# Kernel optimization log

Hardware: AMD Instinct MI355X
Metric: run time of the kernel (lower is better)

The kernel has to match this reference:

```python
import jax, jax.numpy as jnp
import numpy as np

N_NODES = 10000
N_MOTIFS = 2500          # N_NODES / subgraph_size(=4)
N_AUG = N_NODES + N_MOTIFS
N_EDGES = 500000
NFEAT = 512
NHID = 128


def setup_inputs() -> dict:
    key = jax.random.key(0)
    ks = jax.random.split(key, 14)
    s = 0.05  # param init scale
    return {
        "x": jax.random.normal(ks[0], (N_NODES, NFEAT), jnp.float32),
        "edge_index": jax.random.randint(ks[1], (2, N_EDGES), 0, N_AUG, jnp.int64),
        "motif_list": jax.random.randint(ks[2], (N_MOTIFS, 4), 0, N_NODES, jnp.int64),
        "W1": jax.random.normal(ks[3], (NFEAT, 2 * NHID), jnp.float32) * s,
        "a_src1": jax.random.normal(ks[4], (2 * NHID,), jnp.float32) * s,
        "a_dst1": jax.random.normal(ks[5], (2 * NHID,), jnp.float32) * s,
        "b1": jnp.zeros((2 * NHID,), jnp.float32),
        "W2": jax.random.normal(ks[6], (2 * NHID, NHID), jnp.float32) * s,
        "a_src2": jax.random.normal(ks[7], (NHID,), jnp.float32) * s,
        "a_dst2": jax.random.normal(ks[8], (NHID,), jnp.float32) * s,
        "b2": jnp.zeros((NHID,), jnp.float32),
        "W_lin": jax.random.normal(ks[9], (NFEAT, NHID), jnp.float32) * s,  # torch Linear(nhid, nfeat) weight
        "b_lin": jnp.zeros((NFEAT,), jnp.float32),
    }


def gat_layer(x, src, dst, W, a_s, a_d, b, n):
    """Single-head GATConv (PyG semantics): edge-softmax attention over dst."""
    h = x @ W                                              # [n, out]
    alpha_s = h @ a_s                                      # [n]
    alpha_d = h @ a_d                                      # [n]
    e = jax.nn.leaky_relu(alpha_s[src] + alpha_d[dst], 0.2)  # [E]
    m = jax.ops.segment_max(e, dst, num_segments=n)        # stable softmax per dst
    w = jnp.exp(e - m[dst])
    denom = jax.ops.segment_sum(w, dst, num_segments=n)
    coef = w / (denom[dst] + 1e-16)                        # [E]
    out = jax.ops.segment_sum(coef[:, None] * h[src], dst, num_segments=n)
    return out + b


def reference(x, edge_index, motif_list, W1, a_src1, a_dst1, b1,
              W2, a_src2, a_dst2, b2, W_lin, b_lin):
    n = x.shape[0] + motif_list.shape[0]
    # augmented features: mean of each motif's node features appended as motif nodes
    x_aug = jnp.concatenate([x, jnp.mean(x[motif_list], axis=1)], axis=0)  # [N_AUG, F]
    # augmented edge list + self loops (GATConv adds self loops)
    loops = jnp.arange(n, dtype=edge_index.dtype)
    src = jnp.concatenate([edge_index[0], loops])
    dst = jnp.concatenate([edge_index[1], loops])
    h1 = gat_layer(x_aug, src, dst, W1, a_src1, a_dst1, b1, n)   # [N_AUG, 2*NHID]
    h2 = gat_layer(h1, src, dst, W2, a_src2, a_dst2, b2, n)      # [N_AUG, NHID]
    rec_adj = jax.nn.sigmoid(h2 @ h2.T)                          # [N_AUG, N_AUG]
    rec_feature = jax.nn.sigmoid(h2 @ W_lin.T + b_lin)           # [N_AUG, NFEAT]
    return (rec_feature, rec_adj)
```

## Files before the change

kernel.cpp:

```cpp
#include <hip/hip_runtime.h>

typedef unsigned short u16;
typedef __attribute__((ext_vector_type(8))) short short8;
typedef __attribute__((ext_vector_type(4))) float f32x4;

#define N_NODES 10000
#define N_MOTIFS 2500
#define N_AUG   12500
#define N_EDGES 500000
#define E_TOT   512500
#define NFEAT   512
#define NH1     256
#define NH2     128

__device__ __forceinline__ float b2f(u16 u){ return __uint_as_float(((unsigned)u) << 16); }
__device__ __forceinline__ u16 f2b(float f){
  unsigned x = __float_as_uint(f);
  x += 0x7fffu + ((x >> 16) & 1u);
  return (u16)(x >> 16);
}

__global__ void k_zero(int* p, int n){
  int i = blockIdx.x * blockDim.x + threadIdx.x;
  if (i < n) p[i] = 0;
}

__global__ void k_xaug(const float* __restrict__ x, const int* __restrict__ motif,
                       u16* __restrict__ xb){
  int gid = blockIdx.x * blockDim.x + threadIdx.x;
  int row = gid >> 6;
  int c   = (gid & 63) << 3;
  if (row >= N_AUG) return;
  float v[8];
  if (row < N_NODES){
    const float* s = &x[(size_t)row * NFEAT + c];
    #pragma unroll
    for (int k = 0; k < 8; ++k) v[k] = s[k];
  } else {
    int m = row - N_NODES;
    const float* p0 = &x[(size_t)motif[m*4+0] * NFEAT + c];
    const float* p1 = &x[(size_t)motif[m*4+1] * NFEAT + c];
    const float* p2 = &x[(size_t)motif[m*4+2] * NFEAT + c];
    const float* p3 = &x[(size_t)motif[m*4+3] * NFEAT + c];
    #pragma unroll
    for (int k = 0; k < 8; ++k) v[k] = (p0[k] + p1[k] + p2[k] + p3[k]) * 0.25f;
  }
  short8 o;
  #pragma unroll
  for (int k = 0; k < 8; ++k) o[k] = (short)f2b(v[k]);
  *(short8*)&xb[(size_t)row * NFEAT + c] = o;
}

__global__ void k_tr(const float* __restrict__ in, u16* __restrict__ out, int R, int C){
  int i = blockIdx.x * blockDim.x + threadIdx.x;
  if (i >= R * C) return;
  int r = i / C, c = i - r * C;
  out[(size_t)c * R + r] = f2b(in[i]);
}

__global__ void k_cvt(const float* __restrict__ in, u16* __restrict__ out, int n){
  int i = blockIdx.x * blockDim.x + threadIdx.x;
  if (i < n) out[i] = f2b(in[i]);
}

__global__ void k_hist(const int* __restrict__ ei, int* __restrict__ cnt){
  int i = blockIdx.x * blockDim.x + threadIdx.x;
  if (i >= E_TOT) return;
  int d = (i < N_EDGES) ? ei[N_EDGES + i] : (i - N_EDGES);
  atomicAdd(&cnt[d], 1);
}

__global__ void k_scan(const int* __restrict__ cnt, int* __restrict__ offs, int* __restrict__ cur){
  __shared__ int part[1024];
  int t = threadIdx.x;
  const int CH = 13;
  int base = t * CH;
  int s = 0;
  for (int i = 0; i < CH; ++i){ int idx = base + i; if (idx < N_AUG) s += cnt[idx]; }
  part[t] = s;
  __syncthreads();
  for (int off = 1; off < 1024; off <<= 1){
    int v = 0;
    if (t >= off) v = part[t - off];
    __syncthreads();
    if (t >= off) part[t] += v;
    __syncthreads();
  }
  int run = (t == 0) ? 0 : part[t - 1];
  for (int i = 0; i < CH; ++i){
    int idx = base + i;
    if (idx <= N_AUG){
      offs[idx] = run;
      if (idx < N_AUG){ cur[idx] = run; run += cnt[idx]; }
    }
  }
}

__global__ void k_scatter(const int* __restrict__ ei, int* __restrict__ cur, int* __restrict__ srcs){
  int i = blockIdx.x * blockDim.x + threadIdx.x;
  if (i >= E_TOT) return;
  int s, d;
  if (i < N_EDGES){ s = ei[i]; d = ei[N_EDGES + i]; } else { s = i - N_EDGES; d = s; }
  int pos = atomicAdd(&cur[d], 1);
  srcs[pos] = s;
}

template<int DIM>
__global__ void k_alpha(const float* __restrict__ h, const float* __restrict__ avs,
                        const float* __restrict__ avd, float* __restrict__ oS, float* __restrict__ oD){
  __shared__ float shS[8], shD[8];
  int n = blockIdx.x, t = threadIdx.x;
  int lane = t & 63, wid = t >> 6;
  float hv = h[(size_t)n * DIM + t];
  float s = hv * avs[t];
  float d = hv * avd[t];
  #pragma unroll
  for (int o = 32; o; o >>= 1){ s += __shfl_down(s, o); d += __shfl_down(d, o); }
  if (lane == 0){ shS[wid] = s; shD[wid] = d; }
  __syncthreads();
  if (t == 0){
    float ss = 0.f, dd = 0.f;
    for (int i = 0; i < DIM/64; ++i){ ss += shS[i]; dd += shD[i]; }
    oS[n] = ss; oD[n] = dd;
  }
}

template<int DIM>
__global__ void k_agg(const int* __restrict__ offs, const int* __restrict__ srcs,
                      const float* __restrict__ aS, const float* __restrict__ aD,
                      const float* __restrict__ hb, const float* __restrict__ bias,
                      u16* __restrict__ hout){
  __shared__ float rsh[8];
  __shared__ float wsh[128];
  __shared__ int   ssh[128];
  int d = blockIdx.x, t = threadIdx.x;
  int lane = t & 63, wid = t >> 6;
  const int NW = DIM / 64;
  int r0 = offs[d], r1 = offs[d + 1];
  float adv = aD[d];

  float mx = -3.0e38f;
  for (int j = r0 + t; j < r1; j += DIM){
    float e = aS[srcs[j]] + adv;
    e = (e >= 0.f) ? e : 0.2f * e;
    mx = fmaxf(mx, e);
  }
  #pragma unroll
  for (int o = 32; o; o >>= 1) mx = fmaxf(mx, __shfl_down(mx, o));
  if (lane == 0) rsh[wid] = mx;
  __syncthreads();
  if (t == 0){ float v = rsh[0]; for (int i = 1; i < NW; ++i) v = fmaxf(v, rsh[i]); rsh[0] = v; }
  __syncthreads();
  mx = rsh[0];
  __syncthreads();

  float sm = 0.f;
  for (int j = r0 + t; j < r1; j += DIM){
    float e = aS[srcs[j]] + adv;
    e = (e >= 0.f) ? e : 0.2f * e;
    sm += __expf(e - mx);
  }
  #pragma unroll
  for (int o = 32; o; o >>= 1) sm += __shfl_down(sm, o);
  if (lane == 0) rsh[wid] = sm;
  __syncthreads();
  if (t == 0){ float v = rsh[0]; for (int i = 1; i < NW; ++i) v += rsh[i]; rsh[0] = v; }
  __syncthreads();
  sm = rsh[0];

  float acc = 0.f;
  for (int base = r0; base < r1; base += 128){
    int cntE = min(128, r1 - base);
    __syncthreads();
    for (int j = t; j < cntE; j += DIM){
      int s = srcs[base + j];
      ssh[j] = s;
      float e = aS[s] + adv;
      e = (e >= 0.f) ? e : 0.2f * e;
      wsh[j] = __expf(e - mx);
    }
    __syncthreads();
    for (int j = 0; j < cntE; ++j)
      acc += wsh[j] * hb[(size_t)ssh[j] * DIM + t];
  }
  float outv = acc / (sm + 1e-16f) + bias[t];
  hout[(size_t)d * DIM + t] = f2b(outv);
}

template<int EPI>
__global__ __launch_bounds__(256) void k_gemm(
    const u16* __restrict__ A, const u16* __restrict__ B,
    float* __restrict__ C, const float* __restrict__ bias,
    int M, int N, int K){
  __shared__ u16 As[128][72];
  __shared__ u16 Bs[128][72];
  int t = threadIdx.x;
  int lane = t & 63, wid = t >> 6;
  int wm = wid >> 1, wn = wid & 1;
  int m0 = blockIdx.y * 128, n0 = blockIdx.x * 128;

  f32x4 acc[4][4];
  #pragma unroll
  for (int i = 0; i < 4; ++i)
    #pragma unroll
    for (int j = 0; j < 4; ++j)
      acc[i][j] = {0.f, 0.f, 0.f, 0.f};

  for (int k0 = 0; k0 < K; k0 += 64){
    __syncthreads();
    #pragma unroll
    for (int i = 0; i < 4; ++i){
      int id = t + i * 256;
      int r = id >> 3, c = (id & 7) << 3;
      int gm = m0 + r; if (gm >= M) gm = M - 1;
      int gn = n0 + r; if (gn >= N) gn = N - 1;
      *(short8*)&As[r][c] = *(const short8*)&A[(size_t)gm * K + k0 + c];
      *(short8*)&Bs[r][c] = *(const short8*)&B[(size_t)gn * K + k0 + c];
    }
    __syncthreads();
    #pragma unroll
    for (int kk = 0; kk < 2; ++kk){
      int kof = kk * 32 + (lane >> 4) * 8;
      short8 af[4], bfr[4];
      #pragma unroll
      for (int mi = 0; mi < 4; ++mi) af[mi]  = *(const short8*)&As[wm*64 + mi*16 + (lane & 15)][kof];
      #pragma unroll
      for (int ni = 0; ni < 4; ++ni) bfr[ni] = *(const short8*)&Bs[wn*64 + ni*16 + (lane & 15)][kof];
      #pragma unroll
      for (int mi = 0; mi < 4; ++mi)
        #pragma unroll
        for (int ni = 0; ni < 4; ++ni)
          acc[mi][ni] = __builtin_amdgcn_mfma_f32_16x16x32_bf16(af[mi], bfr[ni], acc[mi][ni], 0, 0, 0);
    }
  }

  #pragma unroll
  for (int mi = 0; mi < 4; ++mi)
    #pragma unroll
    for (int ni = 0; ni < 4; ++ni){
      int gn = n0 + wn*64 + ni*16 + (lane & 15);
      if (gn >= N) continue;
      #pragma unroll
      for (int r = 0; r < 4; ++r){
        int gm = m0 + wm*64 + mi*16 + (lane >> 4)*4 + r;
        if (gm >= M) continue;
        float v = acc[mi][ni][r];
        if (EPI == 2) v += bias[gn];
        if (EPI >= 1) v = 1.f / (1.f + __expf(-v));
        C[(size_t)gm * N + gn] = v;
      }
    }
}


extern "C" void kernel_launch(void* const* d_in, const int* in_sizes, int n_in,
                              void* d_out, int out_size, void* d_ws, size_t ws_size,
                              hipStream_t stream){
  const float* x    = (const float*)d_in[0];
  const int*   ei   = (const int*)d_in[1];
  const int*   mot  = (const int*)d_in[2];
  const float* W1   = (const float*)d_in[3];
  const float* a_s1 = (const float*)d_in[4];
  const float* a_d1 = (const float*)d_in[5];
  const float* b1   = (const float*)d_in[6];
  const float* W2   = (const float*)d_in[7];
  const float* a_s2 = (const float*)d_in[8];
  const float* a_d2 = (const float*)d_in[9];
  const float* b2   = (const float*)d_in[10];
  const float* Wl   = (const float*)d_in[11];
  const float* bl   = (const float*)d_in[12];

  char* p = (char*)d_ws;
  auto alloc = [&](size_t bytes){ void* r = (void*)p; p += (bytes + 255) & ~(size_t)255; return r; };
  u16*   xaugb = (u16*)alloc((size_t)N_AUG * NFEAT * 2);
  u16*   W1T   = (u16*)alloc((size_t)NH1 * NFEAT * 2);
  u16*   W2T   = (u16*)alloc((size_t)NH2 * NH1 * 2);
  u16*   Wlb   = (u16*)alloc((size_t)NFEAT * NH2 * 2);
  float* h1pre = (float*)alloc((size_t)N_AUG * NH1 * 4);
  u16*   h1out = (u16*)alloc((size_t)N_AUG * NH1 * 2);
  float* h2pre = (float*)alloc((size_t)N_AUG * NH2 * 4);
  u16*   h2b   = (u16*)alloc((size_t)N_AUG * NH2 * 2);
  float* aS    = (float*)alloc((size_t)N_AUG * 4);
  float* aD    = (float*)alloc((size_t)N_AUG * 4);
  int*   cnt   = (int*)alloc((size_t)(N_AUG + 8) * 4);
  int*   offs  = (int*)alloc((size_t)(N_AUG + 8) * 4);
  int*   cur   = (int*)alloc((size_t)(N_AUG + 8) * 4);
  int*   srcs  = (int*)alloc((size_t)E_TOT * 4);

  float* out_feat = (float*)d_out;
  float* out_adj  = out_feat + (size_t)N_AUG * NFEAT;

  k_zero<<<(N_AUG + 8 + 255) / 256, 256, 0, stream>>>(cnt, N_AUG + 8);
  k_xaug<<<(N_AUG * 64 + 255) / 256, 256, 0, stream>>>(x, mot, xaugb);
  k_tr<<<(NFEAT * NH1 + 255) / 256, 256, 0, stream>>>(W1, W1T, NFEAT, NH1);
  k_tr<<<(NH1 * NH2 + 255) / 256, 256, 0, stream>>>(W2, W2T, NH1, NH2);
  k_cvt<<<(NFEAT * NH2 + 255) / 256, 256, 0, stream>>>(Wl, Wlb, NFEAT * NH2);
  k_hist<<<(E_TOT + 255) / 256, 256, 0, stream>>>(ei, cnt);
  k_scan<<<1, 1024, 0, stream>>>(cnt, offs, cur);
  k_scatter<<<(E_TOT + 255) / 256, 256, 0, stream>>>(ei, cur, srcs);

  { dim3 g(NH1 / 128, 98); k_gemm<0><<<g, 256, 0, stream>>>(xaugb, W1T, h1pre, nullptr, N_AUG, NH1, NFEAT); }
  k_alpha<NH1><<<N_AUG, NH1, 0, stream>>>(h1pre, a_s1, a_d1, aS, aD);
  k_agg<NH1><<<N_AUG, NH1, 0, stream>>>(offs, srcs, aS, aD, h1pre, b1, h1out);

  { dim3 g(1, 98); k_gemm<0><<<g, 256, 0, stream>>>(h1out, W2T, h2pre, nullptr, N_AUG, NH2, NH1); }
  k_alpha<NH2><<<N_AUG, NH2, 0, stream>>>(h2pre, a_s2, a_d2, aS, aD);
  k_agg<NH2><<<N_AUG, NH2, 0, stream>>>(offs, srcs, aS, aD, h2pre, b2, h2b);

  { dim3 g(NFEAT / 128, 98); k_gemm<2><<<g, 256, 0, stream>>>(h2b, Wlb, out_feat, bl, N_AUG, NFEAT, NH2); }
  { dim3 g(98, 98);          k_gemm<1><<<g, 256, 0, stream>>>(h2b, h2b, out_adj, nullptr, N_AUG, N_AUG, NH2); }
}
```

Measured before the change: 464.2 us.

## Store GAT hidden features in bf16, pack aggregation to two columns per thread

The projection GEMMs now write bf16 instead of fp32. The alpha and aggregation kernels read bf16, and each aggregation thread handles two packed columns with half as many threads, replacing block reductions with wave shuffles where possible. The weight prep kernels are merged into one launch, and the sigmoid outputs use nontemporal stores. This cuts gather bandwidth in the edge aggregation and some launch overhead, at the cost of lower precision in the attention scores and the aggregated features.

New measurement: 705.7 us, median of 5. +52.0%, slower.

```diff
diff --git a/kernel.cpp b/kernel.cpp
--- a/kernel.cpp
+++ b/kernel.cpp
@@ -1,6 +1,7 @@
 #include <hip/hip_runtime.h>
 
 typedef unsigned short u16;
+typedef unsigned int   u32;
 typedef __attribute__((ext_vector_type(8))) short short8;
 typedef __attribute__((ext_vector_type(4))) float f32x4;
 
@@ -13,16 +14,38 @@
 #define NH1     256
 #define NH2     128
 
-__device__ __forceinline__ float b2f(u16 u){ return __uint_as_float(((unsigned)u) << 16); }
+__device__ __forceinline__ float b2f(u16 u){ return __uint_as_float(((u32)u) << 16); }
 __device__ __forceinline__ u16 f2b(float f){
-  unsigned x = __float_as_uint(f);
+  u32 x = __float_as_uint(f);
   x += 0x7fffu + ((x >> 16) & 1u);
   return (u16)(x >> 16);
 }
 
-__global__ void k_zero(int* p, int n){
+#define PREP_Z   (N_AUG + 8)
+#define PREP_W1  (NFEAT * NH1)
+#define PREP_W2  (NH1 * NH2)
+#define PREP_WL  (NFEAT * NH2)
+#define PREP_TOT (PREP_Z + PREP_W1 + PREP_W2 + PREP_WL)
+
+__global__ void k_prep(const float* __restrict__ W1, const float* __restrict__ W2,
+                       const float* __restrict__ Wl, int* __restrict__ cnt,
+                       u16* __restrict__ W1T, u16* __restrict__ W2T, u16* __restrict__ Wlb){
   int i = blockIdx.x * blockDim.x + threadIdx.x;
-  if (i < n) p[i] = 0;
+  if (i < PREP_Z){ cnt[i] = 0; return; }
+  i -= PREP_Z;
+  if (i < PREP_W1){
+    int r = i / NH1, c = i - r * NH1;
+    W1T[(size_t)c * NFEAT + r] = f2b(W1[i]);
+    return;
+  }
+  i -= PREP_W1;
+  if (i < PREP_W2){
+    int r = i / NH2, c = i - r * NH2;
+    W2T[(size_t)c * NH1 + r] = f2b(W2[i]);
+    return;
+  }
+  i -= PREP_W2;
+  if (i < PREP_WL) Wlb[i] = f2b(Wl[i]);
 }
 
 __global__ void k_xaug(const float* __restrict__ x, const int* __restrict__ motif,
@@ -49,18 +72,6 @@
   #pragma unroll
   for (int k = 0; k < 8; ++k) o[k] = (short)f2b(v[k]);
   *(short8*)&xb[(size_t)row * NFEAT + c] = o;
-}
-
-__global__ void k_tr(const float* __restrict__ in, u16* __restrict__ out, int R, int C){
-  int i = blockIdx.x * blockDim.x + threadIdx.x;
-  if (i >= R * C) return;
-  int r = i / C, c = i - r * C;
-  out[(size_t)c * R + r] = f2b(in[i]);
-}
-
-__global__ void k_cvt(const float* __restrict__ in, u16* __restrict__ out, int n){
-  int i = blockIdx.x * blockDim.x + threadIdx.x;
-  if (i < n) out[i] = f2b(in[i]);
 }
 
 __global__ void k_hist(const int* __restrict__ ei, int* __restrict__ cnt){
@@ -106,12 +117,12 @@
 }
 
 template<int DIM>
-__global__ void k_alpha(const float* __restrict__ h, const float* __restrict__ avs,
+__global__ void k_alpha(const u16* __restrict__ h, const float* __restrict__ avs,
                         const float* __restrict__ avd, float* __restrict__ oS, float* __restrict__ oD){
   __shared__ float shS[8], shD[8];
   int n = blockIdx.x, t = threadIdx.x;
   int lane = t & 63, wid = t >> 6;
-  float hv = h[(size_t)n * DIM + t];
+  float hv = b2f(h[(size_t)n * DIM + t]);
   float s = hv * avs[t];
   float d = hv * avd[t];
   #pragma unroll
@@ -120,59 +131,65 @@
   __syncthreads();
   if (t == 0){
     float ss = 0.f, dd = 0.f;
+    #pragma unroll
     for (int i = 0; i < DIM/64; ++i){ ss += shS[i]; dd += shD[i]; }
     oS[n] = ss; oD[n] = dd;
   }
 }
 
-template<int DIM>
-__global__ void k_agg(const int* __restrict__ offs, const int* __restrict__ srcs,
-                      const float* __restrict__ aS, const float* __restrict__ aD,
-                      const float* __restrict__ hb, const float* __restrict__ bias,
-                      u16* __restrict__ hout){
-  __shared__ float rsh[8];
+template<int DIM, int T>
+__global__ __launch_bounds__(T) void k_agg(
+    const int* __restrict__ offs, const int* __restrict__ srcs,
+    const float* __restrict__ aS, const float* __restrict__ aD,
+    const u16* __restrict__ hb, const float* __restrict__ bias,
+    u16* __restrict__ hout){
+  constexpr int NW = T / 64;
+  __shared__ float rsh[2];
   __shared__ float wsh[128];
   __shared__ int   ssh[128];
   int d = blockIdx.x, t = threadIdx.x;
   int lane = t & 63, wid = t >> 6;
-  const int NW = DIM / 64;
   int r0 = offs[d], r1 = offs[d + 1];
   float adv = aD[d];
 
   float mx = -3.0e38f;
-  for (int j = r0 + t; j < r1; j += DIM){
+  for (int j = r0 + t; j < r1; j += T){
     float e = aS[srcs[j]] + adv;
     e = (e >= 0.f) ? e : 0.2f * e;
     mx = fmaxf(mx, e);
   }
   #pragma unroll
   for (int o = 32; o; o >>= 1) mx = fmaxf(mx, __shfl_down(mx, o));
-  if (lane == 0) rsh[wid] = mx;
-  __syncthreads();
-  if (t == 0){ float v = rsh[0]; for (int i = 1; i < NW; ++i) v = fmaxf(v, rsh[i]); rsh[0] = v; }
-  __syncthreads();
-  mx = rsh[0];
-  __syncthreads();
+  if constexpr (NW == 2){
+    if (lane == 0) rsh[wid] = mx;
+    __syncthreads();
+    mx = fmaxf(rsh[0], rsh[1]);
+    __syncthreads();
+  } else {
+    mx = __shfl(mx, 0);
+  }
 
   float sm = 0.f;
-  for (int j = r0 + t; j < r1; j += DIM){
+  for (int j = r0 + t; j < r1; j += T){
     float e = aS[srcs[j]] + adv;
     e = (e >= 0.f) ? e : 0.2f * e;
     sm += __expf(e - mx);
   }
   #pragma unroll
   for (int o = 32; o; o >>= 1) sm += __shfl_down(sm, o);
-  if (lane == 0) rsh[wid] = sm;
-  __syncthreads();
-  if (t == 0){ float v = rsh[0]; for (int i = 1; i < NW; ++i) v += rsh[i]; rsh[0] = v; }
-  __syncthreads();
-  sm = rsh[0];
-
-  float acc = 0.f;
+  if constexpr (NW == 2){
+    if (lane == 0) rsh[wid] = sm;
+    __syncthreads();
+    sm = rsh[0] + rsh[1];
+  } else {
+    sm = __shfl(sm, 0);
+  }
+
+  float a0 = 0.f, a1 = 0.f;
   for (int base = r0; base < r1; base += 128){
     int cntE = min(128, r1 - base);
     __syncthreads();
-    for (int j = t; j < cntE; j += DIM){
+    for (int j = t; j < cntE; j += T){
       int s = srcs[base + j];
       ssh[j] = s;
       float e = aS[s] + adv;
@@ -180,17 +197,25 @@
       wsh[j] = __expf(e - mx);
     }
     __syncthreads();
-    for (int j = 0; j < cntE; ++j)
-      acc += wsh[j] * hb[(size_t)ssh[j] * DIM + t];
-  }
-  float outv = acc / (sm + 1e-16f) + bias[t];
-  hout[(size_t)d * DIM + t] = f2b(outv);
+    #pragma unroll 4
+    for (int j = 0; j < cntE; ++j){
+      u32 v = *(const u32*)&hb[(size_t)ssh[j] * DIM + 2*t];
+      float w = wsh[j];
+      a0 = fmaf(w, b2f((u16)(v & 0xffffu)), a0);
+      a1 = fmaf(w, b2f((u16)(v >> 16)), a1);
+    }
+  }
+  float inv = 1.f / (sm + 1e-16f);
+  float o0 = a0 * inv + bias[2*t];
+  float o1 = a1 * inv + bias[2*t + 1];
+  u32 pv = (u32)f2b(o0) | ((u32)f2b(o1) << 16);
+  *(u32*)&hout[(size_t)d * DIM + 2*t] = pv;
 }
 
 template<int EPI>
 __global__ __launch_bounds__(256) void k_gemm(
     const u16* __restrict__ A, const u16* __restrict__ B,
-    float* __restrict__ C, const float* __restrict__ bias,
+    void* __restrict__ Cv, const float* __restrict__ bias,
     int M, int N, int K){
   __shared__ u16 As[128][72];
   __shared__ u16 Bs[128][72];
@@ -245,13 +270,16 @@
         int gm = m0 + wm*64 + mi*16 + (lane >> 4)*4 + r;
         if (gm >= M) continue;
         float v = acc[mi][ni][r];
-        if (EPI == 2) v += bias[gn];
-        if (EPI >= 1) v = 1.f / (1.f + __expf(-v));
-        C[(size_t)gm * N + gn] = v;
+        if (EPI == 0){
+          ((u16*)Cv)[(size_t)gm * N + gn] = f2b(v);
+        } else {
+          if (EPI == 2) v += bias[gn];
+          v = 1.f / (1.f + __expf(-v));
+          __builtin_nontemporal_store(v, &((float*)Cv)[(size_t)gm * N + gn]);
+        }
       }
     }
 }
-
 
 extern "C" void kernel_launch(void* const* d_in, const int* in_sizes, int n_in,
                               void* d_out, int out_size, void* d_ws, size_t ws_size,
@@ -276,10 +304,10 @@
   u16*   W1T   = (u16*)alloc((size_t)NH1 * NFEAT * 2);
   u16*   W2T   = (u16*)alloc((size_t)NH2 * NH1 * 2);
   u16*   Wlb   = (u16*)alloc((size_t)NFEAT * NH2 * 2);
-  float* h1pre = (float*)alloc((size_t)N_AUG * NH1 * 4);
+  u16*   h1b   = (u16*)alloc((size_t)N_AUG * NH1 * 2);
   u16*   h1out = (u16*)alloc((size_t)N_AUG * NH1 * 2);
-  float* h2pre = (float*)alloc((size_t)N_AUG * NH2 * 4);
   u16*   h2b   = (u16*)alloc((size_t)N_AUG * NH2 * 2);
+  u16*   h2o   = (u16*)alloc((size_t)N_AUG * NH2 * 2);
   float* aS    = (float*)alloc((size_t)N_AUG * 4);
   float* aD    = (float*)alloc((size_t)N_AUG * 4);
   int*   cnt   = (int*)alloc((size_t)(N_AUG + 8) * 4);
@@ -290,23 +318,20 @@
   float* out_feat = (float*)d_out;
   float* out_adj  = out_feat + (size_t)N_AUG * NFEAT;
 
-  k_zero<<<(N_AUG + 8 + 255) / 256, 256, 0, stream>>>(cnt, N_AUG + 8);
+  k_prep<<<(PREP_TOT + 255) / 256, 256, 0, stream>>>(W1, W2, Wl, cnt, W1T, W2T, Wlb);
   k_xaug<<<(N_AUG * 64 + 255) / 256, 256, 0, stream>>>(x, mot, xaugb);
-  k_tr<<<(NFEAT * NH1 + 255) / 256, 256, 0, stream>>>(W1, W1T, NFEAT, NH1);
-  k_tr<<<(NH1 * NH2 + 255) / 256, 256, 0, stream>>>(W2, W2T, NH1, NH2);
-  k_cvt<<<(NFEAT * NH2 + 255) / 256, 256, 0, stream>>>(Wl, Wlb, NFEAT * NH2);
   k_hist<<<(E_TOT + 255) / 256, 256, 0, stream>>>(ei, cnt);
   k_scan<<<1, 1024, 0, stream>>>(cnt, offs, cur);
   k_scatter<<<(E_TOT + 255) / 256, 256, 0, stream>>>(ei, cur, srcs);
 
-  { dim3 g(NH1 / 128, 98); k_gemm<0><<<g, 256, 0, stream>>>(xaugb, W1T, h1pre, nullptr, N_AUG, NH1, NFEAT); }
-  k_alpha<NH1><<<N_AUG, NH1, 0, stream>>>(h1pre, a_s1, a_d1, aS, aD);
-  k_agg<NH1><<<N_AUG, NH1, 0, stream>>>(offs, srcs, aS, aD, h1pre, b1, h1out);
-
-  { dim3 g(1, 98); k_gemm<0><<<g, 256, 0, stream>>>(h1out, W2T, h2pre, nullptr, N_AUG, NH2, NH1); }
-  k_alpha<NH2><<<N_AUG, NH2, 0, stream>>>(h2pre, a_s2, a_d2, aS, aD);
-  k_agg<NH2><<<N_AUG, NH2, 0, stream>>>(offs, srcs, aS, aD, h2pre, b2, h2b);
-
-  { dim3 g(NFEAT / 128, 98); k_gemm<2><<<g, 256, 0, stream>>>(h2b, Wlb, out_feat, bl, N_AUG, NFEAT, NH2); }
-  { dim3 g(98, 98);          k_gemm<1><<<g, 256, 0, stream>>>(h2b, h2b, out_adj, nullptr, N_AUG, N_AUG, NH2); }
-}
+  { dim3 g(NH1 / 128, 98); k_gemm<0><<<g, 256, 0, stream>>>(xaugb, W1T, h1b, nullptr, N_AUG, NH1, NFEAT); }
+  k_alpha<NH1><<<N_AUG, NH1, 0, stream>>>(h1b, a_s1, a_d1, aS, aD);
+  k_agg<NH1, 128><<<N_AUG, 128, 0, stream>>>(offs, srcs, aS, aD, h1b, b1, h1out);
+
+  { dim3 g(1, 98); k_gemm<0><<<g, 256, 0, stream>>>(h1out, W2T, h2b, nullptr, N_AUG, NH2, NH1); }
+  k_alpha<NH2><<<N_AUG, NH2, 0, stream>>>(h2b, a_s2, a_d2, aS, aD);
+  k_agg<NH2, 64><<<N_AUG, 64, 0, stream>>>(offs, srcs, aS, aD, h2b, b2, h2o);
+
+  { dim3 g(NFEAT / 128, 98); k_gemm<2><<<g, 256, 0, stream>>>(h2o, Wlb, out_feat, bl, N_AUG, NFEAT, NH2); }
+  { dim3 g(98, 98);          k_gemm<1><<<g, 256, 0, stream>>>(h2o, h2o, out_adj, nullptr, N_AUG, N_AUG, NH2); }
+}
```
